# Optimization experiments

Hardware: AMD Instinct MI355X
Metric: run time of the kernel (lower is better)

Reference implementation:

```python
import jax, jax.numpy as jnp
import numpy as np
import math

B, D, N, T, H = 16, 64, 200, 48, 8
DK = D // H
EPS = 1e-5


def layer_norm(x, g, b):
    m = jnp.mean(x, axis=-1, keepdims=True)
    v = jnp.var(x, axis=-1, keepdims=True)
    return (x - m) * jax.lax.rsqrt(v + EPS) * g + b


def conv1x3(x, w, b):
    # x: (B, D, N, T), w: (D, D, 1, 3) 'same' padding along T
    y = jax.lax.conv_general_dilated(
        x, w, window_strides=(1, 1), padding=((0, 0), (1, 1)),
        dimension_numbers=('NCHW', 'OIHW', 'NCHW'))
    return y + b[None, :, None, None]


def setup_inputs() -> dict:
    key = jax.random.key(0)
    ks = jax.random.split(key, 12)
    s = 1.0 / math.sqrt(D)
    inp = {
        'x': jax.random.normal(ks[0], (B, D, N, T), jnp.float32),
        'support_matrix': jax.random.uniform(ks[1], (N, N), jnp.float32) / N,
        'Wq': jax.random.normal(ks[2], (D, D, 1, 3), jnp.float32) * s,
        'bq': jnp.zeros((D,), jnp.float32),
        'Wk': jax.random.normal(ks[3], (D, D, 1, 3), jnp.float32) * s,
        'bk': jnp.zeros((D,), jnp.float32),
        'W1': jax.random.normal(ks[4], (D, D), jnp.float32) * s,
        'b1': jnp.zeros((D,), jnp.float32),
        'W2': jax.random.normal(ks[5], (D, D), jnp.float32) * s,
        'b2': jnp.zeros((D,), jnp.float32),
        'Theta': jax.random.normal(ks[6], (D, D), jnp.float32) * s,
        'g0': jnp.ones((D,), jnp.float32),
        'beta0': jnp.zeros((D,), jnp.float32),
        'g1': jnp.ones((D,), jnp.float32),
        'beta1': jnp.zeros((D,), jnp.float32),
    }
    return inp


def temporal_attn(x, Wq, bq, Wk, bk, W1, b1, W2, b2):
    # x: (B, D, N, T)
    q = conv1x3(x, Wq, bq).reshape(B, H, DK, N, T).transpose(0, 3, 1, 4, 2)  # (B,N,h,T,dk)
    k = conv1x3(x, Wk, bk).reshape(B, H, DK, N, T).transpose(0, 3, 1, 4, 2)
    xp = x.transpose(0, 2, 3, 1)  # (B,N,T,D)
    v = (xp @ W1.T + b1).reshape(B, N, T, H, DK).transpose(0, 1, 3, 2, 4)  # (B,N,h,T,dk)
    scores = jnp.einsum('bnhtd,bnhsd->bnhts', q, k) / math.sqrt(DK)
    p = jax.nn.softmax(scores, axis=-1)
    out = jnp.einsum('bnhts,bnhsd->bnhtd', p, v)
    out = out.transpose(0, 1, 3, 2, 4).reshape(B, N, T, D)
    return out @ W2.T + b2


def spatial_gcn(x, adj, Theta):
    # x: (B,N,T,D) -> per-timestep spatial attention + adjacency-weighted GCN
    xt = x.transpose(0, 2, 1, 3)  # (B,T,N,D)
    score = jnp.einsum('btnf,btmf->btnm', xt, xt) / math.sqrt(D)
    att = jax.nn.softmax(score, axis=-1) / math.sqrt(D)
    agg = jnp.einsum('btnm,btmf->btnf', adj[None, None] * att, xt)
    out = jax.nn.relu(agg @ Theta.T)  # (B,T,N,D)
    return out.transpose(0, 2, 1, 3)  # (B,N,T,D)


def reference(x, support_matrix, Wq, bq, Wk, bk, W1, b1, W2, b2, Theta,
              g0, beta0, g1, beta1):
    t_out = temporal_attn(x, Wq, bq, Wk, bk, W1, b1, W2, b2)
    h = x.transpose(0, 2, 3, 1) + layer_norm(t_out, g0, beta0)  # (B,N,T,D)
    s_out = spatial_gcn(h, support_matrix, Theta)
    return h + layer_norm(s_out, g1, beta1)
```

## Files before the change

### kernel.cpp

```cpp
#include <hip/hip_runtime.h>
#include <hip/hip_bf16.h>

typedef unsigned short u16t;

namespace {

constexpr int kB = 16, kD = 64, kN = 200, kT = 48, kH = 8;
constexpr float kEps = 1e-5f;

typedef __attribute__((ext_vector_type(8))) __bf16 bf16x8;
typedef __attribute__((ext_vector_type(4))) float f32x4;
union B8 { int4 i; bf16x8 v; u16t u[8]; };

__device__ __forceinline__ u16t f2bfu(float f) {
  union { __hip_bfloat16 h; u16t u; } c; c.h = __float2bfloat16(f); return c.u;
}
__device__ __forceinline__ unsigned pk2(float a, float b) {
  return (unsigned)f2bfu(a) | ((unsigned)f2bfu(b) << 16);
}

constexpr int kWqOff = 0;
constexpr int kWkOff = 12288;
constexpr int kW1Off = 24576;
constexpr int kW2Off = 28672;
constexpr int kThOff = 32768;
constexpr size_t kWsWeightBytes = 73728;
constexpr size_t kHBytes = (size_t)kB * kN * kT * kD * 4;

__global__ void k0_prep(const float* __restrict__ Wq, const float* __restrict__ Wk,
                        const float* __restrict__ W1, const float* __restrict__ W2,
                        const float* __restrict__ Theta, u16t* __restrict__ ws) {
  const int tid = blockIdx.x * 256 + threadIdx.x;
  const int stride = gridDim.x * 256;
  for (int idx = tid; idx < 64 * 192; idx += stride) {
    const int row = idx / 192, rem = idx % 192;
    const int tap = rem >> 6, c = rem & 63;
    const int src = row * 192 + c * 3 + tap;
    ws[kWqOff + idx] = f2bfu(Wq[src]);
    ws[kWkOff + idx] = f2bfu(Wk[src]);
  }
  for (int idx = tid; idx < 4096; idx += stride) {
    ws[kW1Off + idx] = f2bfu(W1[idx]);
    ws[kW2Off + idx] = f2bfu(W2[idx]);
    ws[kThOff + idx] = f2bfu(Theta[idx]);
  }
}

__global__ __launch_bounds__(256, 4) void k1_temporal(
    const float* __restrict__ x, const u16t* __restrict__ ws,
    const float* __restrict__ bq, const float* __restrict__ bk,
    const float* __restrict__ b1, const float* __restrict__ b2,
    const float* __restrict__ g0, const float* __restrict__ beta0,
    float* __restrict__ hout)
{
  __shared__ __align__(16) float qs[3072];
  __shared__ __align__(16) u16t lds_h[13440];
  u16t* XT  = lds_h;
  u16t* osT = lds_h;
  u16t* QT  = lds_h + 3200;
  u16t* KT  = lds_h + 6272;
  u16t* VTT = lds_h + 9344;

  const int tid = threadIdx.x;
  const int b = blockIdx.x / kN, n = blockIdx.x % kN;
  const int wv = tid >> 6, lane = tid & 63;
  const int c15 = lane & 15, quad = lane >> 4;

  if (tid < 192) {
    const int dp = tid & 31, j = tid >> 5;
    const int d0 = dp * 2;
    const size_t xi = (size_t)b * (kD*kN*kT) + (size_t)d0 * (kN*kT) + (size_t)n * kT + j * 8;
    const float4 a0 = *(const float4*)(x + xi);
    const float4 a1 = *(const float4*)(x + xi + 4);
    const float4 c0 = *(const float4*)(x + xi + kN*kT);
    const float4 c1 = *(const float4*)(x + xi + kN*kT + 4);
    float f0[8] = {a0.x,a0.y,a0.z,a0.w,a1.x,a1.y,a1.z,a1.w};
    float f1[8] = {c0.x,c0.y,c0.z,c0.w,c1.x,c1.y,c1.z,c1.w};
    u16t* bb = XT + (d0 & 7);
    const int blk = d0 >> 3;
    #pragma unroll
    for (int e = 0; e < 8; ++e) {
      const int r = j*8 + e + 1;
      const unsigned pkd = (unsigned)f2bfu(f0[e]) | ((unsigned)f2bfu(f1[e]) << 16);
      *(unsigned*)(bb + r*64 + ((blk + r) & 7) * 8) = pkd;
    }
  } else if (tid < 208) {
    const int g = tid - 192;
    const int rr = (g >> 3) ? 49 : 0, gg = g & 7;
    *(int4*)(XT + rr*64 + gg*8) = make_int4(0,0,0,0);
  }
  if (tid < 128) {
    const int d = tid >> 1, g = tid & 1;
    *(int4*)(VTT + d*64 + (((6 + g + d) & 7) << 3)) = make_int4(0,0,0,0);
  }
  __syncthreads();

  {
    const int dqr = wv*16 + c15;
    B8 aq[6], ak[6], av2[2];
    #pragma unroll
    for (int tap = 0; tap < 3; ++tap)
      #pragma unroll
      for (int ksp = 0; ksp < 2; ++ksp) {
        const int off = dqr*192 + tap*64 + ksp*32 + quad*8;
        aq[tap*2+ksp].i = *(const int4*)(ws + kWqOff + off);
        ak[tap*2+ksp].i = *(const int4*)(ws + kWkOff + off);
      }
    #pragma unroll
    for (int ksp = 0; ksp < 2; ++ksp)
      av2[ksp].i = *(const int4*)(ws + kW1Off + dqr*64 + ksp*32 + quad*8);
    float bqv[4], bkv[4], b1v[4];
    #pragma unroll
    for (int r = 0; r < 4; ++r) {
      const int row = wv*16 + quad*4 + r;
      bqv[r] = bq[row]; bkv[r] = bk[row]; b1v[r] = b1[row];
    }
    const int dbase = wv*16 + quad*4;
    const int dblk = dbase >> 3;
    constexpr float kScale = 0.35355339059327373f;

    for (int i = 0; i < 3; ++i) {
      const int t0 = i * 16;
      B8 bf[3][2];
      #pragma unroll
      for (int tap = 0; tap < 3; ++tap)
        #pragma unroll
        for (int ksp = 0; ksp < 2; ++ksp) {
          const int r = t0 + c15 + tap;
          bf[tap][ksp].i = *(const int4*)(XT + r*64 + (((ksp*4 + quad) + r) & 7)*8);
        }
      f32x4 accq = {0.f,0.f,0.f,0.f}, acck = {0.f,0.f,0.f,0.f}, accv = {0.f,0.f,0.f,0.f};
      #pragma unroll
      for (int tap = 0; tap < 3; ++tap)
        #pragma unroll
        for (int ksp = 0; ksp < 2; ++ksp) {
          accq = __builtin_amdgcn_mfma_f32_16x16x32_bf16(aq[tap*2+ksp].v, bf[tap][ksp].v, accq, 0, 0, 0);
          acck = __builtin_amdgcn_mfma_f32_16x16x32_bf16(ak[tap*2+ksp].v, bf[tap][ksp].v, acck, 0, 0, 0);
        }
      #pragma unroll
      for (int ksp = 0; ksp < 2; ++ksp)
        accv = __builtin_amdgcn_mfma_f32_16x16x32_bf16(av2[ksp].v, bf[1][ksp].v, accv, 0, 0, 0);

      const int t = t0 + c15;
      const int rotq = (dblk + t) & 7;
      const unsigned q01 = pk2((accq[0]+bqv[0])*kScale, (accq[1]+bqv[1])*kScale);
      const unsigned q23 = pk2((accq[2]+bqv[2])*kScale, (accq[3]+bqv[3])*kScale);
      *(int2*)(QT + t*64 + rotq*8 + (quad&1)*4) = make_int2((int)q01, (int)q23);
      const unsigned k01 = pk2(acck[0]+bkv[0], acck[1]+bkv[1]);
      const unsigned k23 = pk2(acck[2]+bkv[2], acck[3]+bkv[3]);
      *(int2*)(KT + t*64 + rotq*8 + (quad&1)*4) = make_int2((int)k01, (int)k23);
      #pragma unroll
      for (int r = 0; r < 4; ++r) {
        const int d = dbase + r;
        VTT[d*64 + ((((t>>3) + d) & 7) << 3) + (t & 7)] = f2bfu(accv[r] + b1v[r]);
      }
    }
  }
  __syncthreads();

  #pragma unroll
  for (int hh = 0; hh < 2; ++hh) {
    const int h = wv*2 + hh;
    B8 vb[2];
    #pragma unroll
    for (int ksp = 0; ksp < 2; ++ksp) {
      if (c15 < 8) {
        const int dr = h*8 + c15;
        vb[ksp].i = *(const int4*)(VTT + dr*64 + (((ksp*4 + quad + dr) & 7) << 3));
      } else vb[ksp].i = make_int4(0,0,0,0);
    }
    #pragma unroll
    for (int nt = 0; nt < 3; ++nt) {
      B8 qb;
      if (quad == 0) {
        const int t = nt*16 + c15;
        qb.i = *(const int4*)(QT + t*64 + (((h + t) & 7) << 3));
      } else qb.i = make_int4(0,0,0,0);
      f32x4 sa[3];
      #pragma unroll
      for (int ms = 0; ms < 3; ++ms) {
        B8 ka;
        if (quad == 0) {
          const int s = ms*16 + c15;
          ka.i = *(const int4*)(KT + s*64 + (((h + s) & 7) << 3));
        } else ka.i = make_int4(0,0,0,0);
        f32x4 z = {0.f,0.f,0.f,0.f};
        sa[ms] = __builtin_amdgcn_mfma_f32_16x16x32_bf16(ka.v, qb.v, z, 0, 0, 0);
      }
      float mx = sa[0][0];
      #pragma unroll
      for (int ms = 0; ms < 3; ++ms)
        #pragma unroll
        for (int r = 0; r < 4; ++r) mx = fmaxf(mx, sa[ms][r]);
      mx = fmaxf(mx, __shfl_xor(mx, 16, 64));
      mx = fmaxf(mx, __shfl_xor(mx, 32, 64));
      float p[3][4]; float es = 0.f;
      #pragma unroll
      for (int ms = 0; ms < 3; ++ms)
        #pragma unroll
        for (int r = 0; r < 4; ++r) { p[ms][r] = __expf(sa[ms][r] - mx); es += p[ms][r]; }
      es += __shfl_xor(es, 16, 64);
      es += __shfl_xor(es, 32, 64);
      const float inv = 1.f / es;
      unsigned pkk[3][2];
      #pragma unroll
      for (int ms = 0; ms < 3; ++ms) {
        pkk[ms][0] = pk2(p[ms][0]*inv, p[ms][1]*inv);
        pkk[ms][1] = pk2(p[ms][2]*inv, p[ms][3]*inv);
      }
      const int srcA = c15 + ((2*(quad & 1)) << 4);
      const int srcB = srcA + 16;
      const unsigned w0A = __shfl((int)pkk[0][0], srcA, 64), w0B = __shfl((int)pkk[1][0], srcA, 64);
      const unsigned w1A = __shfl((int)pkk[0][1], srcA, 64), w1B = __shfl((int)pkk[1][1], srcA, 64);
      const unsigned w2A = __shfl((int)pkk[0][0], srcB, 64), w2B = __shfl((int)pkk[1][0], srcB, 64);
      const unsigned w3A = __shfl((int)pkk[0][1], srcB, 64), w3B = __shfl((int)pkk[1][1], srcB, 64);
      const bool hi = quad >= 2;
      B8 a0;
      a0.i = make_int4((int)(hi ? w0B : w0A), (int)(hi ? w1B : w1A),
                       (int)(hi ? w2B : w2A), (int)(hi ? w3B : w3A));
      const int srcC = (c15 + ((2*quad) << 4)) & 63;
      const int srcD = (srcC + 16) & 63;
      const unsigned y0 = __shfl((int)pkk[2][0], srcC, 64), y1 = __shfl((int)pkk[2][1], srcC, 64);
      const unsigned y2 = __shfl((int)pkk[2][0], srcD, 64), y3 = __shfl((int)pkk[2][1], srcD, 64);
      B8 a1;
      if (quad < 2) a1.i = make_int4((int)y0, (int)y1, (int)y2, (int)y3);
      else          a1.i = make_int4(0,0,0,0);
      f32x4 ov = {0.f,0.f,0.f,0.f};
      ov = __builtin_amdgcn_mfma_f32_16x16x32_bf16(a0.v, vb[0].v, ov, 0, 0, 0);
      ov = __builtin_amdgcn_mfma_f32_16x16x32_bf16(a1.v, vb[1].v, ov, 0, 0, 0);
      if (c15 < 8) {
        #pragma unroll
        for (int r = 0; r < 4; ++r) {
          const int t = nt*16 + quad*4 + r;
          osT[t*64 + (((h + t) & 7) << 3) + c15] = f2bfu(ov[r]);
        }
      }
    }
  }
  __syncthreads();

  {
    const int dqr = wv*16 + c15;
    B8 a2[2];
    #pragma unroll
    for (int ksp = 0; ksp < 2; ++ksp)
      a2[ksp].i = *(const int4*)(ws + kW2Off + dqr*64 + ksp*32 + quad*8);
    float b2v[4];
    #pragma unroll
    for (int r = 0; r < 4; ++r) b2v[r] = b2[wv*16 + quad*4 + r];
    for (int i = 0; i < 3; ++i) {
      const int t0 = i * 16;
      f32x4 acc = {0.f,0.f,0.f,0.f};
      #pragma unroll
      for (int ksp = 0; ksp < 2; ++ksp) {
        const int r = t0 + c15;
        B8 bo; bo.i = *(const int4*)(osT + r*64 + (((ksp*4 + quad) + r) & 7)*8);
        acc = __builtin_amdgcn_mfma_f32_16x16x32_bf16(a2[ksp].v, bo.v, acc, 0, 0, 0);
      }
      #pragma unroll
      for (int r = 0; r < 4; ++r)
        qs[(wv*16 + quad*4 + r)*48 + t0 + c15] = acc[r] + b2v[r];
    }
  }
  __syncthreads();

  float* redm = reinterpret_cast<float*>(lds_h);
  float* redv = redm + 192;
  float* mrs  = redm + 384;
  float* rrs  = redm + 432;
  if (tid < 192) {
    const int t = tid >> 2, grp = tid & 3;
    float sm = 0.f, sq = 0.f;
    #pragma unroll
    for (int i = 0; i < 16; ++i) {
      const float v = qs[(grp*16+i)*48 + t];
      sm += v; sq += v*v;
    }
    redm[t*4+grp] = sm; redv[t*4+grp] = sq;
  }
  __syncthreads();
  if (tid < 48) {
    const int t = tid;
    const float sm = redm[t*4] + redm[t*4+1] + redm[t*4+2] + redm[t*4+3];
    const float sq = redv[t*4] + redv[t*4+1] + redv[t*4+2] + redv[t*4+3];
    const float mean = sm * (1.f/64.f);
    const float var = sq * (1.f/64.f) - mean*mean;
    mrs[t] = mean; rrs[t] = rsqrtf(fmaxf(var, 0.f) + kEps);
  }
  __syncthreads();
  if (tid < 192) {
    const int t = tid >> 2, grp = tid & 3;
    const float mean = mrs[t], rs = rrs[t];
    const size_t base = (((size_t)b*kN + n)*kT + t)*kD + grp*16;
    const float* xp = x + (size_t)b*(kD*kN*kT) + (size_t)n*kT + t;
    #pragma unroll
    for (int i4 = 0; i4 < 4; ++i4) {
      float4 o;
      float* op = (float*)&o;
      #pragma unroll
      for (int e = 0; e < 4; ++e) {
        const int d = grp*16 + i4*4 + e;
        const float tout = qs[d*48 + t];
        const float xv = xp[(size_t)d * (kN*kT)];
        op[e] = xv + (tout - mean)*rs*g0[d] + beta0[d];
      }
      *(float4*)(hout + base + i4*4) = o;
    }
  }
}

__global__ __launch_bounds__(256, 4) void k2_spatial_mfma(
    const float* __restrict__ hsrc, float* __restrict__ hdst,
    const float* __restrict__ adj, const u16t* __restrict__ ws,
    const float* __restrict__ g1, const float* __restrict__ beta1, int nparts)
{
  __shared__ __align__(16) u16t Hs[208*64];
  __shared__ __align__(16) u16t Wb[16*224];
  __shared__ __align__(16) u16t A2[16*64];
  __shared__ float rmax[4][16], rsum[4][16], lnS[4][16], lnQ[4][16];

  const int tid = threadIdx.x;
  int bt, part;
  if (nparts == 2) { bt = blockIdx.x >> 1; part = blockIdx.x & 1; }
  else             { bt = blockIdx.x;      part = 0; }
  const int b = bt / kT, t = bt % kT;
  const int rbBeg = (part == 0) ? 0 : 7;
  const int rbEnd = (nparts == 2 && part == 0) ? 7 : 13;
  const int wv = tid >> 6, lane = tid & 63;
  const int c15 = lane & 15, quad = lane >> 4;
  const int myf = wv*16 + c15;

  const float g1f = g1[myf], be1f = beta1[myf];

  B8 bth[2];
  #pragma unroll
  for (int ksp = 0; ksp < 2; ++ksp)
    bth[ksp].i = *(const int4*)(ws + kThOff + myf*64 + ksp*32 + quad*8);

  for (int idx = tid; idx < kN*8; idx += 256) {
    const int n = idx >> 3, j = idx & 7;
    const float* src = hsrc + (((size_t)b*kN + n)*kT + t)*kD + j*8;
    const float4 p0 = *(const float4*)src, p1 = *(const float4*)(src + 4);
    B8 p;
    p.u[0]=f2bfu(p0.x); p.u[1]=f2bfu(p0.y); p.u[2]=f2bfu(p0.z); p.u[3]=f2bfu(p0.w);
    p.u[4]=f2bfu(p1.x); p.u[5]=f2bfu(p1.y); p.u[6]=f2bfu(p1.z); p.u[7]=f2bfu(p1.w);
    *(int4*)(Hs + n*64 + (((j + n) & 7) << 3)) = p.i;
  }
  if (tid < 64) {
    *(int4*)(Hs + (200 + (tid >> 3))*64 + ((tid & 7) << 3)) = make_int4(0,0,0,0);
  }
  for (int idx = tid; idx < (16*224)/8; idx += 256)
    *(int4*)(Wb + idx*8) = make_int4(0,0,0,0);
  __syncthreads();

  const int dA = wv*16 + c15;
  B8 ahi[7];
  #pragma unroll
  for (int ksp = 0; ksp < 6; ++ksp) {
    const int m0 = ksp*32 + quad*8;
    #pragma unroll
    for (int j = 0; j < 8; ++j) {
      const int m = m0 + j;
      ahi[ksp].u[j] = Hs[m*64 + ((((dA>>3) + m) & 7) << 3) + (dA & 7)];
    }
  }
  if (quad == 0) {
    #pragma unroll
    for (int j = 0; j < 8; ++j) {
      const int m = 192 + j;
      ahi[6].u[j] = Hs[m*64 + ((((dA>>3) + m) & 7) << 3) + (dA & 7)];
    }
  } else {
    ahi[6].i = make_int4(0, 0, 0, 0);
  }

  for (int rb = rbBeg; rb < rbEnd; ++rb) {
    const int n0 = rb * 16;

    B8 afr[2];
    #pragma unroll
    for (int ksp = 0; ksp < 2; ++ksp) {
      const int row = n0 + c15;
      afr[ksp].i = *(const int4*)(Hs + row*64 + (((ksp*4 + quad + row) & 7) << 3));
    }
    f32x4 cs[3];
    #pragma unroll
    for (int i = 0; i < 3; ++i) {
      const int mt = wv + 4*i;
      f32x4 acc = {0.f, 0.f, 0.f, 0.f};
      #pragma unroll
      for (int ksp = 0; ksp < 2; ++ksp) {
        const int row = mt*16 + c15;
        B8 bfr; bfr.i = *(const int4*)(Hs + row*64 + (((ksp*4 + quad + row) & 7) << 3));
        acc = __builtin_amdgcn_mfma_f32_16x16x32_bf16(afr[ksp].v, bfr.v, acc, 0, 0, 0);
      }
      cs[i] = acc;
    }
    const bool has4 = (wv == 0);
    f32x4 cs3 = {0.f, 0.f, 0.f, 0.f};
    if (has4) {
      #pragma unroll
      for (int ksp = 0; ksp < 2; ++ksp) {
        const int row = 192 + c15;
        B8 bfr; bfr.i = *(const int4*)(Hs + row*64 + (((ksp*4 + quad + row) & 7) << 3));
        cs3 = __builtin_amdgcn_mfma_f32_16x16x32_bf16(afr[ksp].v, bfr.v, cs3, 0, 0, 0);
      }
    }

    float mxr[4], smr[4];
    #pragma unroll
    for (int r = 0; r < 4; ++r) {
      cs[0][r] *= 0.125f; cs[1][r] *= 0.125f; cs[2][r] *= 0.125f; cs3[r] *= 0.125f;
      float m = fmaxf(fmaxf(cs[0][r], cs[1][r]), cs[2][r]);
      if (has4 && c15 < 8) m = fmaxf(m, cs3[r]);
      mxr[r] = m;
    }
    #pragma unroll
    for (int off = 1; off <= 8; off <<= 1)
      #pragma unroll
      for (int r = 0; r < 4; ++r) mxr[r] = fmaxf(mxr[r], __shfl_xor(mxr[r], off, 64));
    #pragma unroll
    for (int r = 0; r < 4; ++r) {
      cs[0][r] = __expf(fminf(cs[0][r] - mxr[r], 0.f));
      cs[1][r] = __expf(fminf(cs[1][r] - mxr[r], 0.f));
      cs[2][r] = __expf(fminf(cs[2][r] - mxr[r], 0.f));
      cs3[r]   = (has4 && c15 < 8) ? __expf(fminf(cs3[r] - mxr[r], 0.f)) : 0.f;
      smr[r] = cs[0][r] + cs[1][r] + cs[2][r] + cs3[r];
    }
    #pragma unroll
    for (int off = 1; off <= 8; off <<= 1)
      #pragma unroll
      for (int r = 0; r < 4; ++r) smr[r] += __shfl_xor(smr[r], off, 64);
    if (c15 == 0) {
      #pragma unroll
      for (int r = 0; r < 4; ++r) { rmax[wv][quad*4 + r] = mxr[r]; rsum[wv][quad*4 + r] = smr[r]; }
    }
    __syncthreads();
    #pragma unroll
    for (int r = 0; r < 4; ++r) {
      const int rr = quad*4 + r;
      const float m0 = rmax[0][rr], m1 = rmax[1][rr], m2 = rmax[2][rr], m3 = rmax[3][rr];
      const float M = fmaxf(fmaxf(m0, m1), fmaxf(m2, m3));
      const float tot = rsum[0][rr]*__expf(m0 - M) + rsum[1][rr]*__expf(m1 - M)
                      + rsum[2][rr]*__expf(m2 - M) + rsum[3][rr]*__expf(m3 - M);
      const float fw = __expf(fminf(mxr[r] - M, 0.f));
      const float inv = 0.125f / fmaxf(tot, 1e-20f) * fw;
      const int n = n0 + rr;
      const bool vrow = (n < kN);
      const int na = vrow ? n : (kN - 1);
      #pragma unroll
      for (int i = 0; i < 3; ++i) {
        const int m = (wv + 4*i)*16 + c15;
        const float w = vrow ? cs[i][r] * inv * adj[(size_t)na*kN + m] : 0.f;
        Wb[rr*224 + (((m >> 3) + rr) % 28)*8 + (m & 7)] = f2bfu(w);
      }
      if (has4 && c15 < 8) {
        const int m = 192 + c15;
        const float w = vrow ? cs3[r] * inv * adj[(size_t)na*kN + m] : 0.f;
        Wb[rr*224 + (((m >> 3) + rr) % 28)*8 + (m & 7)] = f2bfu(w);
      }
    }
    __syncthreads();

    f32x4 ag = {0.f, 0.f, 0.f, 0.f};
    #pragma unroll
    for (int ksp = 0; ksp < 7; ++ksp) {
      B8 bw; bw.i = *(const int4*)(Wb + c15*224 + ((ksp*4 + quad + c15) % 28)*8);
      ag = __builtin_amdgcn_mfma_f32_16x16x32_bf16(ahi[ksp].v, bw.v, ag, 0, 0, 0);
    }
    {
      const int dbase = wv*16 + quad*4;
      #pragma unroll
      for (int r = 0; r < 4; ++r) {
        const int d = dbase + r;
        A2[c15*64 + (((d >> 3) + c15) & 7)*8 + (d & 7)] = f2bfu(ag[r]);
      }
    }
    __syncthreads();

    f32x4 o = {0.f, 0.f, 0.f, 0.f};
    #pragma unroll
    for (int ksp = 0; ksp < 2; ++ksp) {
      B8 a; a.i = *(const int4*)(A2 + c15*64 + (((ksp*4 + quad + c15) & 7) << 3));
      o = __builtin_amdgcn_mfma_f32_16x16x32_bf16(a.v, bth[ksp].v, o, 0, 0, 0);
    }
    float vr[4], ps[4], pq[4];
    #pragma unroll
    for (int r = 0; r < 4; ++r) {
      vr[r] = fmaxf(o[r], 0.f);
      ps[r] = vr[r]; pq[r] = vr[r]*vr[r];
    }
    #pragma unroll
    for (int off = 1; off <= 8; off <<= 1)
      #pragma unroll
      for (int r = 0; r < 4; ++r) {
        ps[r] += __shfl_xor(ps[r], off, 64);
        pq[r] += __shfl_xor(pq[r], off, 64);
      }
    if (c15 == 0) {
      #pragma unroll
      for (int r = 0; r < 4; ++r) { lnS[wv][quad*4+r] = ps[r]; lnQ[wv][quad*4+r] = pq[r]; }
    }
    __syncthreads();
    #pragma unroll
    for (int r = 0; r < 4; ++r) {
      const int rr = quad*4 + r, n = n0 + rr;
      const float S = lnS[0][rr] + lnS[1][rr] + lnS[2][rr] + lnS[3][rr];
      const float Q = lnQ[0][rr] + lnQ[1][rr] + lnQ[2][rr] + lnQ[3][rr];
      const float mean = S * (1.f/64.f);
      const float var = Q * (1.f/64.f) - mean*mean;
      const float rs = rsqrtf(fmaxf(var, 0.f) + kEps);
      if (n < kN) {
        const float sout = (vr[r] - mean)*rs*g1f + be1f;
        const size_t oi = (((size_t)b*kN + n)*kT + t)*kD + myf;
        hdst[oi] = hsrc[oi] + sout;
      }
    }
  }
}

}

extern "C" void kernel_launch(void* const* d_in, const int* in_sizes, int n_in,
                              void* d_out, int out_size, void* d_ws, size_t ws_size,
                              hipStream_t stream) {
  const float* x     = (const float*)d_in[0];
  const float* adj   = (const float*)d_in[1];
  const float* Wq    = (const float*)d_in[2];
  const float* bq    = (const float*)d_in[3];
  const float* Wk    = (const float*)d_in[4];
  const float* bk    = (const float*)d_in[5];
  const float* W1    = (const float*)d_in[6];
  const float* b1    = (const float*)d_in[7];
  const float* W2    = (const float*)d_in[8];
  const float* b2    = (const float*)d_in[9];
  const float* Theta = (const float*)d_in[10];
  const float* g0    = (const float*)d_in[11];
  const float* beta0 = (const float*)d_in[12];
  const float* g1    = (const float*)d_in[13];
  const float* beta1 = (const float*)d_in[14];

  u16t* wsb = (u16t*)d_ws;

  const bool split = ws_size >= kWsWeightBytes + kHBytes;
  float* hbuf = split ? (float*)((char*)d_ws + kWsWeightBytes) : (float*)d_out;
  const int nparts = split ? 2 : 1;

  k0_prep<<<dim3(48), dim3(256), 0, stream>>>(Wq, Wk, W1, W2, Theta, wsb);
  k1_temporal<<<dim3(kB*kN), dim3(256), 0, stream>>>(
      x, wsb, bq, bk, b1, b2, g0, beta0, hbuf);
  k2_spatial_mfma<<<dim3(kB*kT*nparts), dim3(256), 0, stream>>>(
      hbuf, (float*)d_out, adj, wsb, g1, beta1, nparts);
}
```

Before: 293.1 us.

## Process 32 spatial rows per iteration and drop split-block mode in spatial kernel

The spatial GCN kernel now handles two 16-row tiles per loop iteration. The B-operand fragments of H and the barriers are shared across both tiles, and adjacency values are prefetched into registers before the softmax. The two-part split over (b,t) and the separate workspace copy of h are removed, so h is updated in place in the output buffer with one block per (b,t). The aim is to halve the number of barrier rounds, overlap the adjacency loads, and avoid the extra workspace traffic. The cost is higher register and LDS pressure (launch bounds lowered to 3 waves per EU) and half as many blocks, which reduces parallelism.

```diff
diff --git a/kernel.cpp b/kernel.cpp
--- a/kernel.cpp
+++ b/kernel.cpp
@@ -24,8 +24,6 @@
 constexpr int kW1Off = 24576;
 constexpr int kW2Off = 28672;
 constexpr int kThOff = 32768;
-constexpr size_t kWsWeightBytes = 73728;
-constexpr size_t kHBytes = (size_t)kB * kN * kT * kD * 4;
 
 __global__ void k0_prep(const float* __restrict__ Wq, const float* __restrict__ Wk,
                         const float* __restrict__ W1, const float* __restrict__ W2,
@@ -309,23 +307,18 @@
   }
 }
 
-__global__ __launch_bounds__(256, 4) void k2_spatial_mfma(
-    const float* __restrict__ hsrc, float* __restrict__ hdst,
-    const float* __restrict__ adj, const u16t* __restrict__ ws,
-    const float* __restrict__ g1, const float* __restrict__ beta1, int nparts)
+__global__ __launch_bounds__(256, 3) void k2_spatial_mfma(
+    float* __restrict__ hio, const float* __restrict__ adj,
+    const u16t* __restrict__ ws, const float* __restrict__ g1,
+    const float* __restrict__ beta1)
 {
   __shared__ __align__(16) u16t Hs[208*64];
-  __shared__ __align__(16) u16t Wb[16*224];
-  __shared__ __align__(16) u16t A2[16*64];
-  __shared__ float rmax[4][16], rsum[4][16], lnS[4][16], lnQ[4][16];
+  __shared__ __align__(16) u16t Wb[32*224];
+  __shared__ __align__(16) u16t A2[32*64];
+  __shared__ float rmax[4][32], rsum[4][32], lnS[4][32], lnQ[4][32];
 
   const int tid = threadIdx.x;
-  int bt, part;
-  if (nparts == 2) { bt = blockIdx.x >> 1; part = blockIdx.x & 1; }
-  else             { bt = blockIdx.x;      part = 0; }
-  const int b = bt / kT, t = bt % kT;
-  const int rbBeg = (part == 0) ? 0 : 7;
-  const int rbEnd = (nparts == 2 && part == 0) ? 7 : 13;
+  const int b = blockIdx.x / kT, t = blockIdx.x % kT;
   const int wv = tid >> 6, lane = tid & 63;
   const int c15 = lane & 15, quad = lane >> 4;
   const int myf = wv*16 + c15;
@@ -339,7 +332,7 @@
 
   for (int idx = tid; idx < kN*8; idx += 256) {
     const int n = idx >> 3, j = idx & 7;
-    const float* src = hsrc + (((size_t)b*kN + n)*kT + t)*kD + j*8;
+    const float* src = hio + (((size_t)b*kN + n)*kT + t)*kD + j*8;
     const float4 p0 = *(const float4*)src, p1 = *(const float4*)(src + 4);
     B8 p;
     p.u[0]=f2bfu(p0.x); p.u[1]=f2bfu(p0.y); p.u[2]=f2bfu(p0.z); p.u[3]=f2bfu(p0.w);
@@ -349,7 +342,7 @@
   if (tid < 64) {
     *(int4*)(Hs + (200 + (tid >> 3))*64 + ((tid & 7) << 3)) = make_int4(0,0,0,0);
   }
-  for (int idx = tid; idx < (16*224)/8; idx += 256)
+  for (int idx = tid; idx < (32*224)/8; idx += 256)
     *(int4*)(Wb + idx*8) = make_int4(0,0,0,0);
   __syncthreads();
 
@@ -374,146 +367,212 @@
     ahi[6].i = make_int4(0, 0, 0, 0);
   }
 
-  for (int rb = rbBeg; rb < rbEnd; ++rb) {
-    const int n0 = rb * 16;
-
-    B8 afr[2];
+  for (int cc = 0; cc < 7; ++cc) {
+    const int n0 = cc * 32;
+    const bool hasB = (cc < 6);
+    const bool has4 = (wv == 0);
+
+    float adjA[3][4], adjB[3][4];
+    #pragma unroll
+    for (int r = 0; r < 4; ++r) {
+      const int nA = n0 + quad*4 + r;
+      const int naA = (nA < kN) ? nA : (kN - 1);
+      const int nB = n0 + 16 + quad*4 + r;
+      const int naB = (nB < kN) ? nB : (kN - 1);
+      #pragma unroll
+      for (int i = 0; i < 3; ++i) {
+        const int m = (wv + 4*i)*16 + c15;
+        adjA[i][r] = adj[(size_t)naA*kN + m];
+        adjB[i][r] = hasB ? adj[(size_t)naB*kN + m] : 0.f;
+      }
+    }
+
+    B8 afrA[2], afrB[2];
     #pragma unroll
     for (int ksp = 0; ksp < 2; ++ksp) {
-      const int row = n0 + c15;
-      afr[ksp].i = *(const int4*)(Hs + row*64 + (((ksp*4 + quad + row) & 7) << 3));
-    }
-    f32x4 cs[3];
+      const int rowA = n0 + c15;
+      afrA[ksp].i = *(const int4*)(Hs + rowA*64 + (((ksp*4 + quad + rowA) & 7) << 3));
+      if (hasB) {
+        const int rowB = n0 + 16 + c15;
+        afrB[ksp].i = *(const int4*)(Hs + rowB*64 + (((ksp*4 + quad + rowB) & 7) << 3));
+      } else afrB[ksp].i = make_int4(0,0,0,0);
+    }
+    f32x4 csA[3], csB[3];
     #pragma unroll
     for (int i = 0; i < 3; ++i) {
-      const int mt = wv + 4*i;
-      f32x4 acc = {0.f, 0.f, 0.f, 0.f};
+      f32x4 aA = {0.f,0.f,0.f,0.f}, aB = {0.f,0.f,0.f,0.f};
       #pragma unroll
       for (int ksp = 0; ksp < 2; ++ksp) {
-        const int row = mt*16 + c15;
+        const int row = (wv + 4*i)*16 + c15;
         B8 bfr; bfr.i = *(const int4*)(Hs + row*64 + (((ksp*4 + quad + row) & 7) << 3));
-        acc = __builtin_amdgcn_mfma_f32_16x16x32_bf16(afr[ksp].v, bfr.v, acc, 0, 0, 0);
-      }
-      cs[i] = acc;
-    }
-    const bool has4 = (wv == 0);
-    f32x4 cs3 = {0.f, 0.f, 0.f, 0.f};
+        aA = __builtin_amdgcn_mfma_f32_16x16x32_bf16(afrA[ksp].v, bfr.v, aA, 0, 0, 0);
+        if (hasB) aB = __builtin_amdgcn_mfma_f32_16x16x32_bf16(afrB[ksp].v, bfr.v, aB, 0, 0, 0);
+      }
+      csA[i] = aA; csB[i] = aB;
+    }
+    f32x4 cs3A = {0.f,0.f,0.f,0.f}, cs3B = {0.f,0.f,0.f,0.f};
     if (has4) {
       #pragma unroll
       for (int ksp = 0; ksp < 2; ++ksp) {
         const int row = 192 + c15;
         B8 bfr; bfr.i = *(const int4*)(Hs + row*64 + (((ksp*4 + quad + row) & 7) << 3));
-        cs3 = __builtin_amdgcn_mfma_f32_16x16x32_bf16(afr[ksp].v, bfr.v, cs3, 0, 0, 0);
-      }
-    }
-
-    float mxr[4], smr[4];
+        cs3A = __builtin_amdgcn_mfma_f32_16x16x32_bf16(afrA[ksp].v, bfr.v, cs3A, 0, 0, 0);
+        if (hasB) cs3B = __builtin_amdgcn_mfma_f32_16x16x32_bf16(afrB[ksp].v, bfr.v, cs3B, 0, 0, 0);
+      }
+    }
+
+    float mxrA[4], smrA[4], mxrB[4], smrB[4];
     #pragma unroll
     for (int r = 0; r < 4; ++r) {
-      cs[0][r] *= 0.125f; cs[1][r] *= 0.125f; cs[2][r] *= 0.125f; cs3[r] *= 0.125f;
-      float m = fmaxf(fmaxf(cs[0][r], cs[1][r]), cs[2][r]);
-      if (has4 && c15 < 8) m = fmaxf(m, cs3[r]);
-      mxr[r] = m;
+      csA[0][r] *= 0.125f; csA[1][r] *= 0.125f; csA[2][r] *= 0.125f; cs3A[r] *= 0.125f;
+      csB[0][r] *= 0.125f; csB[1][r] *= 0.125f; csB[2][r] *= 0.125f; cs3B[r] *= 0.125f;
+      float mA = fmaxf(fmaxf(csA[0][r], csA[1][r]), csA[2][r]);
+      float mB = fmaxf(fmaxf(csB[0][r], csB[1][r]), csB[2][r]);
+      if (has4 && c15 < 8) { mA = fmaxf(mA, cs3A[r]); mB = fmaxf(mB, cs3B[r]); }
+      mxrA[r] = mA; mxrB[r] = mB;
     }
     #pragma unroll
     for (int off = 1; off <= 8; off <<= 1)
       #pragma unroll
-      for (int r = 0; r < 4; ++r) mxr[r] = fmaxf(mxr[r], __shfl_xor(mxr[r], off, 64));
+      for (int r = 0; r < 4; ++r) {
+        mxrA[r] = fmaxf(mxrA[r], __shfl_xor(mxrA[r], off, 64));
+        mxrB[r] = fmaxf(mxrB[r], __shfl_xor(mxrB[r], off, 64));
+      }
     #pragma unroll
     for (int r = 0; r < 4; ++r) {
-      cs[0][r] = __expf(fminf(cs[0][r] - mxr[r], 0.f));
-      cs[1][r] = __expf(fminf(cs[1][r] - mxr[r], 0.f));
-      cs[2][r] = __expf(fminf(cs[2][r] - mxr[r], 0.f));
-      cs3[r]   = (has4 && c15 < 8) ? __expf(fminf(cs3[r] - mxr[r], 0.f)) : 0.f;
-      smr[r] = cs[0][r] + cs[1][r] + cs[2][r] + cs3[r];
+      csA[0][r] = __expf(fminf(csA[0][r] - mxrA[r], 0.f));
+      csA[1][r] = __expf(fminf(csA[1][r] - mxrA[r], 0.f));
+      csA[2][r] = __expf(fminf(csA[2][r] - mxrA[r], 0.f));
+      cs3A[r]   = (has4 && c15 < 8) ? __expf(fminf(cs3A[r] - mxrA[r], 0.f)) : 0.f;
+      smrA[r] = csA[0][r] + csA[1][r] + csA[2][r] + cs3A[r];
+      csB[0][r] = __expf(fminf(csB[0][r] - mxrB[r], 0.f));
+      csB[1][r] = __expf(fminf(csB[1][r] - mxrB[r], 0.f));
+      csB[2][r] = __expf(fminf(csB[2][r] - mxrB[r], 0.f));
+      cs3B[r]   = (has4 && c15 < 8) ? __expf(fminf(cs3B[r] - mxrB[r], 0.f)) : 0.f;
+      smrB[r] = csB[0][r] + csB[1][r] + csB[2][r] + cs3B[r];
     }
     #pragma unroll
     for (int off = 1; off <= 8; off <<= 1)
       #pragma unroll
-      for (int r = 0; r < 4; ++r) smr[r] += __shfl_xor(smr[r], off, 64);
+      for (int r = 0; r < 4; ++r) {
+        smrA[r] += __shfl_xor(smrA[r], off, 64);
+        smrB[r] += __shfl_xor(smrB[r], off, 64);
+      }
     if (c15 == 0) {
       #pragma unroll
-      for (int r = 0; r < 4; ++r) { rmax[wv][quad*4 + r] = mxr[r]; rsum[wv][quad*4 + r] = smr[r]; }
+      for (int r = 0; r < 4; ++r) {
+        rmax[wv][quad*4 + r] = mxrA[r];      rsum[wv][quad*4 + r] = smrA[r];
+        rmax[wv][16 + quad*4 + r] = mxrB[r]; rsum[wv][16 + quad*4 + r] = smrB[r];
+      }
     }
     __syncthreads();
-    #pragma unroll
-    for (int r = 0; r < 4; ++r) {
-      const int rr = quad*4 + r;
-      const float m0 = rmax[0][rr], m1 = rmax[1][rr], m2 = rmax[2][rr], m3 = rmax[3][rr];
-      const float M = fmaxf(fmaxf(m0, m1), fmaxf(m2, m3));
-      const float tot = rsum[0][rr]*__expf(m0 - M) + rsum[1][rr]*__expf(m1 - M)
-                      + rsum[2][rr]*__expf(m2 - M) + rsum[3][rr]*__expf(m3 - M);
-      const float fw = __expf(fminf(mxr[r] - M, 0.f));
-      const float inv = 0.125f / fmaxf(tot, 1e-20f) * fw;
-      const int n = n0 + rr;
-      const bool vrow = (n < kN);
-      const int na = vrow ? n : (kN - 1);
-      #pragma unroll
-      for (int i = 0; i < 3; ++i) {
-        const int m = (wv + 4*i)*16 + c15;
-        const float w = vrow ? cs[i][r] * inv * adj[(size_t)na*kN + m] : 0.f;
-        Wb[rr*224 + (((m >> 3) + rr) % 28)*8 + (m & 7)] = f2bfu(w);
-      }
-      if (has4 && c15 < 8) {
-        const int m = 192 + c15;
-        const float w = vrow ? cs3[r] * inv * adj[(size_t)na*kN + m] : 0.f;
-        Wb[rr*224 + (((m >> 3) + rr) % 28)*8 + (m & 7)] = f2bfu(w);
+
+    #pragma unroll
+    for (int sub = 0; sub < 2; ++sub) {
+      if (sub == 1 && !hasB) break;
+      #pragma unroll
+      for (int r = 0; r < 4; ++r) {
+        const int rr = quad*4 + r, RR = sub*16 + rr;
+        const float m0 = rmax[0][RR], m1 = rmax[1][RR], m2 = rmax[2][RR], m3 = rmax[3][RR];
+        const float M = fmaxf(fmaxf(m0, m1), fmaxf(m2, m3));
+        const float tot = rsum[0][RR]*__expf(m0 - M) + rsum[1][RR]*__expf(m1 - M)
+                        + rsum[2][RR]*__expf(m2 - M) + rsum[3][RR]*__expf(m3 - M);
+        const float mxr = sub ? mxrB[r] : mxrA[r];
+        const float fw = __expf(fminf(mxr - M, 0.f));
+        const float inv = 0.125f / fmaxf(tot, 1e-20f) * fw;
+        const int n = n0 + RR;
+        const bool vrow = (n < kN);
+        #pragma unroll
+        for (int i = 0; i < 3; ++i) {
+          const int m = (wv + 4*i)*16 + c15;
+          const float cv = sub ? csB[i][r] : csA[i][r];
+          const float av = sub ? adjB[i][r] : adjA[i][r];
+          const float w = vrow ? cv * inv * av : 0.f;
+          Wb[RR*224 + (((m >> 3) + RR) % 28)*8 + (m & 7)] = f2bfu(w);
+        }
+        if (has4 && c15 < 8) {
+          const int m = 192 + c15;
+          const int na = vrow ? n : (kN - 1);
+          const float cv = sub ? cs3B[r] : cs3A[r];
+          const float w = vrow ? cv * inv * adj[(size_t)na*kN + m] : 0.f;
+          Wb[RR*224 + (((m >> 3) + RR) % 28)*8 + (m & 7)] = f2bfu(w);
+        }
       }
     }
     __syncthreads();
 
-    f32x4 ag = {0.f, 0.f, 0.f, 0.f};
-    #pragma unroll
-    for (int ksp = 0; ksp < 7; ++ksp) {
-      B8 bw; bw.i = *(const int4*)(Wb + c15*224 + ((ksp*4 + quad + c15) % 28)*8);
-      ag = __builtin_amdgcn_mfma_f32_16x16x32_bf16(ahi[ksp].v, bw.v, ag, 0, 0, 0);
-    }
-    {
+    #pragma unroll
+    for (int sub = 0; sub < 2; ++sub) {
+      if (sub == 1 && !hasB) break;
+      const int RRrow = sub*16 + c15;
+      f32x4 ag0 = {0.f,0.f,0.f,0.f}, ag1 = {0.f,0.f,0.f,0.f};
+      #pragma unroll
+      for (int ksp = 0; ksp < 7; ++ksp) {
+        B8 bw; bw.i = *(const int4*)(Wb + RRrow*224 + ((ksp*4 + quad + RRrow) % 28)*8);
+        if (ksp & 1) ag1 = __builtin_amdgcn_mfma_f32_16x16x32_bf16(ahi[ksp].v, bw.v, ag1, 0, 0, 0);
+        else         ag0 = __builtin_amdgcn_mfma_f32_16x16x32_bf16(ahi[ksp].v, bw.v, ag0, 0, 0, 0);
+      }
       const int dbase = wv*16 + quad*4;
       #pragma unroll
       for (int r = 0; r < 4; ++r) {
         const int d = dbase + r;
-        A2[c15*64 + (((d >> 3) + c15) & 7)*8 + (d & 7)] = f2bfu(ag[r]);
+        A2[RRrow*64 + (((d >> 3) + RRrow) & 7)*8 + (d & 7)] = f2bfu(ag0[r] + ag1[r]);
       }
     }
     __syncthreads();
 
-    f32x4 o = {0.f, 0.f, 0.f, 0.f};
-    #pragma unroll
-    for (int ksp = 0; ksp < 2; ++ksp) {
-      B8 a; a.i = *(const int4*)(A2 + c15*64 + (((ksp*4 + quad + c15) & 7) << 3));
-      o = __builtin_amdgcn_mfma_f32_16x16x32_bf16(a.v, bth[ksp].v, o, 0, 0, 0);
-    }
-    float vr[4], ps[4], pq[4];
-    #pragma unroll
-    for (int r = 0; r < 4; ++r) {
-      vr[r] = fmaxf(o[r], 0.f);
-      ps[r] = vr[r]; pq[r] = vr[r]*vr[r];
-    }
-    #pragma unroll
-    for (int off = 1; off <= 8; off <<= 1)
-      #pragma unroll
-      for (int r = 0; r < 4; ++r) {
-        ps[r] += __shfl_xor(ps[r], off, 64);
-        pq[r] += __shfl_xor(pq[r], off, 64);
-      }
-    if (c15 == 0) {
-      #pragma unroll
-      for (int r = 0; r < 4; ++r) { lnS[wv][quad*4+r] = ps[r]; lnQ[wv][quad*4+r] = pq[r]; }
+    float vrA[4], vrB[4];
+    #pragma unroll
+    for (int sub = 0; sub < 2; ++sub) {
+      if (sub == 1 && !hasB) break;
+      const int R = sub*16 + c15;
+      f32x4 o = {0.f,0.f,0.f,0.f};
+      #pragma unroll
+      for (int ksp = 0; ksp < 2; ++ksp) {
+        B8 a; a.i = *(const int4*)(A2 + R*64 + (((ksp*4 + quad + R) & 7) << 3));
+        o = __builtin_amdgcn_mfma_f32_16x16x32_bf16(a.v, bth[ksp].v, o, 0, 0, 0);
+      }
+      float ps[4], pq[4];
+      float* vr = sub ? vrB : vrA;
+      #pragma unroll
+      for (int r = 0; r < 4; ++r) {
+        vr[r] = fmaxf(o[r], 0.f);
+        ps[r] = vr[r]; pq[r] = vr[r]*vr[r];
+      }
+      #pragma unroll
+      for (int off = 1; off <= 8; off <<= 1)
+        #pragma unroll
+        for (int r = 0; r < 4; ++r) {
+          ps[r] += __shfl_xor(ps[r], off, 64);
+          pq[r] += __shfl_xor(pq[r], off, 64);
+        }
+      if (c15 == 0) {
+        #pragma unroll
+        for (int r = 0; r < 4; ++r) {
+          lnS[wv][sub*16 + quad*4 + r] = ps[r];
+          lnQ[wv][sub*16 + quad*4 + r] = pq[r];
+        }
+      }
     }
     __syncthreads();
-    #pragma unroll
-    for (int r = 0; r < 4; ++r) {
-      const int rr = quad*4 + r, n = n0 + rr;
-      const float S = lnS[0][rr] + lnS[1][rr] + lnS[2][rr] + lnS[3][rr];
-      const float Q = lnQ[0][rr] + lnQ[1][rr] + lnQ[2][rr] + lnQ[3][rr];
-      const float mean = S * (1.f/64.f);
-      const float var = Q * (1.f/64.f) - mean*mean;
-      const float rs = rsqrtf(fmaxf(var, 0.f) + kEps);
-      if (n < kN) {
-        const float sout = (vr[r] - mean)*rs*g1f + be1f;
-        const size_t oi = (((size_t)b*kN + n)*kT + t)*kD + myf;
-        hdst[oi] = hsrc[oi] + sout;
+
+    #pragma unroll
+    for (int sub = 0; sub < 2; ++sub) {
+      if (sub == 1 && !hasB) break;
+      const float* vr = sub ? vrB : vrA;
+      #pragma unroll
+      for (int r = 0; r < 4; ++r) {
+        const int RR = sub*16 + quad*4 + r, n = n0 + RR;
+        const float S = lnS[0][RR] + lnS[1][RR] + lnS[2][RR] + lnS[3][RR];
+        const float Q = lnQ[0][RR] + lnQ[1][RR] + lnQ[2][RR] + lnQ[3][RR];
+        const float mean = S * (1.f/64.f);
+        const float var = Q * (1.f/64.f) - mean*mean;
+        const float rs = rsqrtf(fmaxf(var, 0.f) + kEps);
+        if (n < kN) {
+          const float sout = (vr[r] - mean)*rs*g1f + be1f;
+          const size_t oi = (((size_t)b*kN + n)*kT + t)*kD + myf;
+          hio[oi] = hio[oi] + sout;
+        }
       }
     }
   }
@@ -540,15 +599,12 @@
   const float* g1    = (const float*)d_in[13];
   const float* beta1 = (const float*)d_in[14];
 
+  float* hbuf = (float*)d_out;
   u16t* wsb = (u16t*)d_ws;
-
-  const bool split = ws_size >= kWsWeightBytes + kHBytes;
-  float* hbuf = split ? (float*)((char*)d_ws + kWsWeightBytes) : (float*)d_out;
-  const int nparts = split ? 2 : 1;
 
   k0_prep<<<dim3(48), dim3(256), 0, stream>>>(Wq, Wk, W1, W2, Theta, wsb);
   k1_temporal<<<dim3(kB*kN), dim3(256), 0, stream>>>(
       x, wsb, bq, bk, b1, b2, g0, beta0, hbuf);
-  k2_spatial_mfma<<<dim3(kB*kT*nparts), dim3(256), 0, stream>>>(
-      hbuf, (float*)d_out, adj, wsb, g1, beta1, nparts);
+  k2_spatial_mfma<<<dim3(kB*kT), dim3(256), 0, stream>>>(
+      hbuf, adj, wsb, g1, beta1);
 }
```

New measurement: 317.6 us. +8.4%, slower.
